# Kernel optimization log

Hardware: AMD Instinct MI355X
Metric: run time of the kernel (lower is better)

The kernel has to match this reference:

```python
import jax, jax.numpy as jnp
import numpy as np

L = 19                      # blur kernel side
K2 = L * L                  # 361 taps
PAD1 = L // 2               # 9 (left/top)
PAD2 = L // 2               # 9 (right/bottom, l odd)


def _sv_blur(x, kernel):
    """Spatially-varying blur: out[b,c,i,j] = sum_k patch_k(x)[b,c,i,j]*kernel[b,k,i,j] / K2.

    Divisor: the torch module always recomputes divisor = fold(unfold(ones)).sum(1)
    (padded size H+18 != 128 init size), and with fold kernel_size=1 this is the
    constant L*L everywhere.
    """
    B, C, H, W = x.shape
    pad = jnp.pad(x, ((0, 0), (0, 0), (PAD1, PAD2), (PAD1, PAD2)), mode='reflect')
    # Extract LxL patches per pixel; single-channel batch of B*C maps, so output
    # channel ordering is row-major over (u, v) kernel offsets, matching torch unfold.
    xr = pad.reshape(B * C, 1, H + PAD1 + PAD2, W + PAD1 + PAD2)
    patches = jax.lax.conv_general_dilated_patches(
        xr, filter_shape=(L, L), window_strides=(1, 1), padding='VALID')  # [B*C, K2, H, W]
    patches = patches.reshape(B, C, K2, H, W)
    out = jnp.einsum('bckhw,bkhw->bchw', patches, kernel)
    return out / jnp.asarray(K2, dtype=out.dtype)


def setup_inputs() -> dict:
    key = jax.random.key(0)
    k1, k2 = jax.random.split(key)
    B, C, H, W = 2, 3, 256, 256
    inp = jax.random.normal(k1, (B, C, H, W), dtype=jnp.float32)
    kernel = jax.random.uniform(k2, (B, K2, H, W), dtype=jnp.float32)
    return {"input": inp, "kernel": kernel}


def reference(input, kernel):
    return _sv_blur(input, kernel)
```

## Files before the change

### kernel.cpp

```cpp
#include <hip/hip_runtime.h>


#define LW     19
#define PAD    9
#define K2     361
#define HH     256
#define WW     256
#define CC     3
#define HW     (HH * WW)

#define TX     16
#define TY     8
#define TPW    4
#define TILE_W (TX * TPW)
#define NCHUNK 5
#define USZ    4
#define RHALO  (TY + USZ - 1)
#define SM_W   84

__global__ __launch_bounds__(128)
void svblur_zero(float* __restrict__ out) {
    int idx = blockIdx.x * 128 + threadIdx.x;
    ((float4*)out)[idx] = make_float4(0.f, 0.f, 0.f, 0.f);
}

__global__ __launch_bounds__(128)
void svblur_main(const float* __restrict__ x,
                 const float* __restrict__ ker,
                 float* __restrict__ out) {
    __shared__ float tile[CC][RHALO][SM_W];

    const int tx    = threadIdx.x;
    const int ty    = threadIdx.y;
    const int tid   = ty * TX + tx;
    const int j0    = blockIdx.x * TILE_W;
    const int i0    = blockIdx.y * TY;
    const int bz    = blockIdx.z;
    const int b     = bz / NCHUNK;
    const int chunk = bz - b * NCHUNK;
    const int u0    = chunk * USZ;
    const int usz   = (chunk == NCHUNK - 1) ? (LW - u0) : USZ;

    const float* xb = x + (size_t)b * CC * HW;
    for (int idx = tid; idx < CC * RHALO * SM_W; idx += TX * TY) {
        int c  = idx / (RHALO * SM_W);
        int rm = idx - c * (RHALO * SM_W);
        int r  = rm / SM_W;
        int cc = rm - r * SM_W;
        int gr = i0 + u0 + r - PAD;
        gr = gr < 0 ? -gr : (gr >= HH ? 2 * HH - 2 - gr : gr);
        int gc = j0 + cc - PAD;
        gc = gc < 0 ? -gc : (gc >= WW ? 2 * WW - 2 - gc : gc);
        ((float*)tile)[idx] = xb[(c * HH + gr) * WW + gc];
    }
    __syncthreads();

    const int jt = tx * TPW;
    const int i  = i0 + ty;
    const int j  = j0 + jt;

    float acc[CC][TPW];
    #pragma unroll
    for (int c = 0; c < CC; ++c)
        #pragma unroll
        for (int p = 0; p < TPW; ++p) acc[c][p] = 0.f;

    for (int uu = 0; uu < usz; ++uu) {
        float xr[CC][24];
        #pragma unroll
        for (int c = 0; c < CC; ++c) {
            const float4* rp = (const float4*)&tile[c][ty + uu][jt];
            #pragma unroll
            for (int q = 0; q < 6; ++q) {
                float4 v4 = rp[q];
                xr[c][q * 4 + 0] = v4.x;
                xr[c][q * 4 + 1] = v4.y;
                xr[c][q * 4 + 2] = v4.z;
                xr[c][q * 4 + 3] = v4.w;
            }
        }
        const float4* kb4 = (const float4*)(ker
            + (size_t)(b * K2 + (u0 + uu) * LW) * HW + (size_t)i * WW + j);
        #pragma unroll
        for (int v = 0; v < LW; ++v) {
            float4 kv = kb4[(size_t)v * (HW / 4)];
            #pragma unroll
            for (int c = 0; c < CC; ++c) {
                acc[c][0] = fmaf(xr[c][v + 0], kv.x, acc[c][0]);
                acc[c][1] = fmaf(xr[c][v + 1], kv.y, acc[c][1]);
                acc[c][2] = fmaf(xr[c][v + 2], kv.z, acc[c][2]);
                acc[c][3] = fmaf(xr[c][v + 3], kv.w, acc[c][3]);
            }
        }
    }

    const float s = 1.0f / (float)K2;
    #pragma unroll
    for (int c = 0; c < CC; ++c) {
        float* op = out + ((size_t)(b * CC + c) * HH + i) * WW + j;
        #pragma unroll
        for (int p = 0; p < TPW; ++p) atomicAdd(op + p, acc[c][p] * s);
    }
}

extern "C" void kernel_launch(void* const* d_in, const int* in_sizes, int n_in,
                              void* d_out, int out_size, void* d_ws, size_t ws_size,
                              hipStream_t stream) {
    const float* x   = (const float*)d_in[0];
    const float* ker = (const float*)d_in[1];
    float* out       = (float*)d_out;

    svblur_zero<<<393216 / 4 / 128, 128, 0, stream>>>(out);

    dim3 grid(WW / TILE_W, HH / TY, 2 * NCHUNK);
    dim3 block(TX, TY, 1);
    svblur_main<<<grid, block, 0, stream>>>(x, ker, out);
}
```

Measured before the change: 279.1 us.

## Split kernel rows across warps in-block and reduce via LDS instead of atomics

Replaces the cross-block split of the 19 kernel rows, which needed global atomics and a separate zeroing kernel, with an in-block split over 8 warp slices. Each slice handles a subset of kernel rows, then partial sums go to shared memory and are reduced and written directly. This removes the zero-fill launch and the atomic traffic. In exchange it adds a larger halo tile, smaller spatial tiles and an extra block-level reduction with a sync.

```diff
diff --git a/kernel.cpp b/kernel.cpp
--- a/kernel.cpp
+++ b/kernel.cpp
@@ -9,45 +9,36 @@
 #define CC     3
 #define HW     (HH * WW)
 
-#define TX     16
-#define TY     8
+#define TX     8
+#define TY     4
+#define NS     8
 #define TPW    4
 #define TILE_W (TX * TPW)
-#define NCHUNK 5
-#define USZ    4
-#define RHALO  (TY + USZ - 1)
-#define SM_W   84
+#define SM_H   (TY + LW - 1)
+#define SM_W   52
 
-__global__ __launch_bounds__(128)
-void svblur_zero(float* __restrict__ out) {
-    int idx = blockIdx.x * 128 + threadIdx.x;
-    ((float4*)out)[idx] = make_float4(0.f, 0.f, 0.f, 0.f);
-}
-
-__global__ __launch_bounds__(128)
+__global__ __launch_bounds__(256, 4)
 void svblur_main(const float* __restrict__ x,
                  const float* __restrict__ ker,
                  float* __restrict__ out) {
-    __shared__ float tile[CC][RHALO][SM_W];
+    __shared__ float tile[CC][SM_H][SM_W];
+    __shared__ float partials[NS * 12 * 32];
 
-    const int tx    = threadIdx.x;
-    const int ty    = threadIdx.y;
-    const int tid   = ty * TX + tx;
-    const int j0    = blockIdx.x * TILE_W;
-    const int i0    = blockIdx.y * TY;
-    const int bz    = blockIdx.z;
-    const int b     = bz / NCHUNK;
-    const int chunk = bz - b * NCHUNK;
-    const int u0    = chunk * USZ;
-    const int usz   = (chunk == NCHUNK - 1) ? (LW - u0) : USZ;
+    const int tx  = threadIdx.x;
+    const int ty  = threadIdx.y;
+    const int s   = threadIdx.z;
+    const int tid = s * 32 + ty * TX + tx;
+    const int j0  = blockIdx.x * TILE_W;
+    const int i0  = blockIdx.y * TY;
+    const int b   = blockIdx.z;
 
     const float* xb = x + (size_t)b * CC * HW;
-    for (int idx = tid; idx < CC * RHALO * SM_W; idx += TX * TY) {
-        int c  = idx / (RHALO * SM_W);
-        int rm = idx - c * (RHALO * SM_W);
+    for (int idx = tid; idx < CC * SM_H * SM_W; idx += 256) {
+        int c  = idx / (SM_H * SM_W);
+        int rm = idx - c * (SM_H * SM_W);
         int r  = rm / SM_W;
         int cc = rm - r * SM_W;
-        int gr = i0 + u0 + r - PAD;
+        int gr = i0 + r - PAD;
         gr = gr < 0 ? -gr : (gr >= HH ? 2 * HH - 2 - gr : gr);
         int gc = j0 + cc - PAD;
         gc = gc < 0 ? -gc : (gc >= WW ? 2 * WW - 2 - gc : gc);
@@ -58,6 +49,8 @@
     const int jt = tx * TPW;
     const int i  = i0 + ty;
     const int j  = j0 + jt;
+    const int u0 = (s * LW) / NS;
+    const int u1 = ((s + 1) * LW) / NS;
 
     float acc[CC][TPW];
     #pragma unroll
@@ -65,11 +58,11 @@
         #pragma unroll
         for (int p = 0; p < TPW; ++p) acc[c][p] = 0.f;
 
-    for (int uu = 0; uu < usz; ++uu) {
+    for (int u = u0; u < u1; ++u) {
         float xr[CC][24];
         #pragma unroll
         for (int c = 0; c < CC; ++c) {
-            const float4* rp = (const float4*)&tile[c][ty + uu][jt];
+            const float4* rp = (const float4*)&tile[c][ty + u][jt];
             #pragma unroll
             for (int q = 0; q < 6; ++q) {
                 float4 v4 = rp[q];
@@ -79,11 +72,11 @@
                 xr[c][q * 4 + 3] = v4.w;
             }
         }
-        const float4* kb4 = (const float4*)(ker
-            + (size_t)(b * K2 + (u0 + uu) * LW) * HW + (size_t)i * WW + j);
+        const float4* kp = (const float4*)(ker
+            + ((size_t)(b * K2 + u * LW)) * HW + (size_t)i * WW + j);
         #pragma unroll
         for (int v = 0; v < LW; ++v) {
-            float4 kv = kb4[(size_t)v * (HW / 4)];
+            float4 kv = kp[(size_t)v * (HW / 4)];
             #pragma unroll
             for (int c = 0; c < CC; ++c) {
                 acc[c][0] = fmaf(xr[c][v + 0], kv.x, acc[c][0]);
@@ -94,12 +87,25 @@
         }
     }
 
-    const float s = 1.0f / (float)K2;
+    const int lane = ty * TX + tx;
     #pragma unroll
-    for (int c = 0; c < CC; ++c) {
-        float* op = out + ((size_t)(b * CC + c) * HH + i) * WW + j;
+    for (int c = 0; c < CC; ++c)
         #pragma unroll
-        for (int p = 0; p < TPW; ++p) atomicAdd(op + p, acc[c][p] * s);
+        for (int p = 0; p < TPW; ++p)
+            partials[(s * 12 + c * 4 + p) * 32 + lane] = acc[c][p];
+    __syncthreads();
+
+    const float sc = 1.0f / (float)K2;
+    for (int r = tid; r < 12 * 32; r += 256) {
+        int cp = r >> 5, ln = r & 31;
+        float sum = 0.f;
+        #pragma unroll
+        for (int ss = 0; ss < NS; ++ss)
+            sum += partials[(ss * 12 + cp) * 32 + ln];
+        int c  = cp >> 2, p = cp & 3;
+        int ii = i0 + (ln >> 3);
+        int jj = j0 + (ln & 7) * TPW + p;
+        out[((size_t)(b * CC + c) * HH + ii) * WW + jj] = sum * sc;
     }
 }
 
@@ -110,9 +116,7 @@
     const float* ker = (const float*)d_in[1];
     float* out       = (float*)d_out;
 
-    svblur_zero<<<393216 / 4 / 128, 128, 0, stream>>>(out);
-
-    dim3 grid(WW / TILE_W, HH / TY, 2 * NCHUNK);
-    dim3 block(TX, TY, 1);
+    dim3 grid(WW / TILE_W, HH / TY, 2);
+    dim3 block(TX, TY, NS);
     svblur_main<<<grid, block, 0, stream>>>(x, ker, out);
 }
```

Measured after the change: 269.2 us, median of 2. 1.04x faster.
